# Performance work log

Hardware: AMD Instinct MI355X
Metric: run time of the kernel (lower is better)

Reference implementation:

```python
import jax, jax.numpy as jnp
import numpy as np

WIN = 9
EPS = 1e-05


def _box_sum(x, win):
    """Depthwise win x win box-filter sum with SAME padding, via two separable 1D convs."""
    C = x.shape[1]
    pad = win // 2
    dn = ('NCHW', 'OIHW', 'NCHW')
    kh = jnp.ones((C, 1, win, 1), dtype=x.dtype)
    kw = jnp.ones((C, 1, 1, win), dtype=x.dtype)
    x = jax.lax.conv_general_dilated(x, kh, (1, 1), [(pad, pad), (0, 0)],
                                     dimension_numbers=dn, feature_group_count=C)
    x = jax.lax.conv_general_dilated(x, kw, (1, 1), [(0, 0), (pad, pad)],
                                     dimension_numbers=dn, feature_group_count=C)
    return x


def setup_inputs() -> dict:
    key = jax.random.key(0)
    k1, k2 = jax.random.split(key)
    B, C, H, W = 32, 4, 512, 512
    y_pred = jax.random.uniform(k1, (B, C, H, W), dtype=jnp.float32)
    y_true = jax.random.uniform(k2, (B, C, H, W), dtype=jnp.float32)
    return {"y_pred": y_pred, "y_true": y_true}


def reference(y_pred, y_true):
    C = y_true.shape[1]
    n = float(WIN * WIN)
    # Stack the 5 moment maps along channels -> one fused box-filter pass.
    stacked = jnp.concatenate(
        [y_true, y_pred, y_true * y_true, y_pred * y_pred, y_true * y_pred], axis=1)
    sums = _box_sum(stacked, WIN)
    sum_I, sum_J, sum_I2, sum_J2, sum_IJ = jnp.split(sums, 5, axis=1)
    mu_I = sum_I / n
    mu_J = sum_J / n
    var_I = sum_I2 / n - mu_I * mu_I
    var_J = sum_J2 / n - mu_J * mu_J
    cov_IJ = sum_IJ / n - mu_I * mu_J
    cc = cov_IJ * cov_IJ / (jnp.maximum(var_I, 0.0) * jnp.maximum(var_J, 0.0) + EPS)
    return -jnp.mean(cc)
```

## Files before the change

kernel.cpp:

```cpp
#include <hip/hip_runtime.h>


#define PAD 4
#define EPS 1e-5f

constexpr int B = 32, C = 4, H = 512, W = 512;
constexpr int ROWS = 32;
constexpr int TPB = 256;
constexpr int CPT = 2;
constexpr int SLOTS = 520;
constexpr int NCHUNK = H / ROWS;
constexpr int NBLK = B * C * NCHUNK;
constexpr int NPART = NBLK * 4;
constexpr float INV_N = 1.0f / 81.0f;

template <bool ADD>
__device__ __forceinline__ void accrow(const float* __restrict__ I,
                                       const float* __restrict__ J,
                                       int r, int x0, float s[5][CPT]) {
    const float2 vi = *(const float2*)(I + (size_t)r * W + x0);
    const float2 vj = *(const float2*)(J + (size_t)r * W + x0);
    float fi[CPT] = {vi.x, vi.y};
    float fj[CPT] = {vj.x, vj.y};
#pragma unroll
    for (int k = 0; k < CPT; ++k) {
        float a = fi[k], b = fj[k];
        if (ADD) {
            s[0][k] += a; s[1][k] += b;
            s[2][k] += a * a; s[3][k] += b * b; s[4][k] += a * b;
        } else {
            s[0][k] -= a; s[1][k] -= b;
            s[2][k] -= a * a; s[3][k] -= b * b; s[4][k] -= a * b;
        }
    }
}

__global__ __launch_bounds__(TPB) void ncc_partial(
        const float* __restrict__ y_pred, const float* __restrict__ y_true,
        float* __restrict__ partial) {
    __shared__ float vs[2][5][SLOTS];

    const int bid = blockIdx.x;
    const int chunk = bid % NCHUNK;
    const int plane = bid / NCHUNK;
    const size_t base = (size_t)plane * H * W;
    const float* I = y_true + base;
    const float* J = y_pred + base;

    const int t = threadIdx.x;
    const int x0 = t * CPT;

    if (t < 2 * PAD) {
        const int sl = (t < PAD) ? t : (512 + t);
#pragma unroll
        for (int b = 0; b < 2; ++b)
#pragma unroll
            for (int ch = 0; ch < 5; ++ch) vs[b][ch][sl] = 0.0f;
    }

    const int y0 = chunk * ROWS;

    float s[5][CPT] = {{0.f, 0.f}, {0.f, 0.f}, {0.f, 0.f}, {0.f, 0.f}, {0.f, 0.f}};

    for (int r = y0 - PAD; r < y0 + PAD; ++r) {
        if (r >= 0 && r < H) accrow<true>(I, J, r, x0, s);
    }

    float acc = 0.0f;

    for (int yo = 0; yo < ROWS; ++yo) {
        const int y = y0 + yo;
        const int rin = y + PAD;
        if (rin < H) accrow<true>(I, J, rin, x0, s);

        float (* const vb)[SLOTS] = vs[yo & 1];
#pragma unroll
        for (int ch = 0; ch < 5; ++ch)
            *(float2*)&vb[ch][x0 + PAD] = make_float2(s[ch][0], s[ch][1]);
        __syncthreads();

        float h[5][CPT];
#pragma unroll
        for (int ch = 0; ch < 5; ++ch) {
            const float* row = vb[ch];
            const float2 r0 = *(const float2*)(row + x0);
            const float2 r1 = *(const float2*)(row + x0 + 2);
            const float2 r2 = *(const float2*)(row + x0 + 4);
            const float2 r3 = *(const float2*)(row + x0 + 6);
            const float2 r4 = *(const float2*)(row + x0 + 8);
            const float s0 = r0.x + r0.y + r1.x + r1.y + r2.x + r2.y +
                             r3.x + r3.y + r4.x;
            h[ch][0] = s0;
            h[ch][1] = s0 + r4.y - r0.x;
        }

#pragma unroll
        for (int k = 0; k < CPT; ++k) {
            const float mI = h[0][k] * INV_N;
            const float mJ = h[1][k] * INV_N;
            const float vI = h[2][k] * INV_N - mI * mI;
            const float vJ = h[3][k] * INV_N - mJ * mJ;
            const float cv = h[4][k] * INV_N - mI * mJ;
            const float den = fmaxf(vI, 0.0f) * fmaxf(vJ, 0.0f) + EPS;
            acc += cv * cv / den;
        }

        const int rout = y - PAD;
        if (rout >= 0) accrow<false>(I, J, rout, x0, s);
    }

#pragma unroll
    for (int off = 32; off > 0; off >>= 1)
        acc += __shfl_down(acc, off, 64);
    if ((t & 63) == 0) partial[bid * 4 + (t >> 6)] = acc;
}

__global__ __launch_bounds__(256) void ncc_final(
        const float* __restrict__ partial, float* __restrict__ out) {
    const int t = threadIdx.x;
    float sum = 0.0f;
    for (int i = t; i < NPART; i += 256) sum += partial[i];
    __shared__ float ws[4];
#pragma unroll
    for (int off = 32; off > 0; off >>= 1)
        sum += __shfl_down(sum, off, 64);
    if ((t & 63) == 0) ws[t >> 6] = sum;
    __syncthreads();
    if (t == 0) {
        const float tot = ws[0] + ws[1] + ws[2] + ws[3];
        out[0] = -tot / (float)((long long)B * C * H * W);
    }
}

extern "C" void kernel_launch(void* const* d_in, const int* in_sizes, int n_in,
                              void* d_out, int out_size, void* d_ws, size_t ws_size,
                              hipStream_t stream) {
    const float* y_pred = (const float*)d_in[0];
    const float* y_true = (const float*)d_in[1];
    float* out = (float*)d_out;
    float* partial = (float*)d_ws;

    ncc_partial<<<NBLK, TPB, 0, stream>>>(y_pred, y_true, partial);
    ncc_final<<<1, 256, 0, stream>>>(partial, out);
}
```

Measured before the change: 115.6 us.

## Map each wavefront to a row chunk, use shuffle-based horizontal box sums

Restructures the kernel so each 64-lane wavefront owns a full 512-wide row strip of 16 rows, with 8 columns per lane. The horizontal 9-tap sum now uses cross-lane shuffles instead of a shared-memory buffer, which removes the per-row __syncthreads. Row loads for the next step are issued early to overlap with compute. It also uses float4 loads, a hardware reciprocal in place of division, and a block-index swizzle across 8 groups. The costs are higher register pressure, more redundant halo row reads from the shorter chunks, and a slightly less precise reciprocal.

```diff
diff --git a/kernel.cpp b/kernel.cpp
--- a/kernel.cpp
+++ b/kernel.cpp
@@ -5,121 +5,158 @@
 #define EPS 1e-5f
 
 constexpr int B = 32, C = 4, H = 512, W = 512;
-constexpr int ROWS = 32;
+constexpr int ROWS = 16;
+constexpr int NCHUNK = H / ROWS;
+constexpr int NTASK = B * C * NCHUNK;
 constexpr int TPB = 256;
-constexpr int CPT = 2;
-constexpr int SLOTS = 520;
-constexpr int NCHUNK = H / ROWS;
-constexpr int NBLK = B * C * NCHUNK;
-constexpr int NPART = NBLK * 4;
+constexpr int WPB = TPB / 64;
+constexpr int NBLK = NTASK / WPB;
 constexpr float INV_N = 1.0f / 81.0f;
 
-template <bool ADD>
-__device__ __forceinline__ void accrow(const float* __restrict__ I,
-                                       const float* __restrict__ J,
-                                       int r, int x0, float s[5][CPT]) {
-    const float2 vi = *(const float2*)(I + (size_t)r * W + x0);
-    const float2 vj = *(const float2*)(J + (size_t)r * W + x0);
-    float fi[CPT] = {vi.x, vi.y};
-    float fj[CPT] = {vj.x, vj.y};
+__device__ __forceinline__ void loadrow(const float* __restrict__ p, int r,
+                                        int x0, float4& a, float4& b) {
+    const float* q = p + (size_t)r * W + x0;
+    a = *(const float4*)q;
+    b = *(const float4*)(q + 4);
+}
+
+__device__ __forceinline__ void unpack8(const float4& a, const float4& b,
+                                        float f[8]) {
+    f[0] = a.x; f[1] = a.y; f[2] = a.z; f[3] = a.w;
+    f[4] = b.x; f[5] = b.y; f[6] = b.z; f[7] = b.w;
+}
+
+__device__ __forceinline__ void hsum(const float sc[8], int lane, float h[8]) {
+    float L[4], R[4];
 #pragma unroll
-    for (int k = 0; k < CPT; ++k) {
-        float a = fi[k], b = fj[k];
-        if (ADD) {
-            s[0][k] += a; s[1][k] += b;
-            s[2][k] += a * a; s[3][k] += b * b; s[4][k] += a * b;
-        } else {
-            s[0][k] -= a; s[1][k] -= b;
-            s[2][k] -= a * a; s[3][k] -= b * b; s[4][k] -= a * b;
-        }
+    for (int k = 0; k < 4; ++k) {
+        L[k] = __shfl_up(sc[4 + k], 1, 64);
+        R[k] = __shfl_down(sc[k], 1, 64);
+    }
+#pragma unroll
+    for (int k = 0; k < 4; ++k) {
+        L[k] = (lane == 0) ? 0.0f : L[k];
+        R[k] = (lane == 63) ? 0.0f : R[k];
+    }
+    float w[16] = {L[0], L[1], L[2], L[3],
+                   sc[0], sc[1], sc[2], sc[3], sc[4], sc[5], sc[6], sc[7],
+                   R[0], R[1], R[2], R[3]};
+    float t = w[0] + w[1] + w[2] + w[3] + w[4] + w[5] + w[6] + w[7] + w[8];
+    h[0] = t;
+#pragma unroll
+    for (int j = 1; j < 8; ++j) {
+        t += w[j + 8] - w[j - 1];
+        h[j] = t;
     }
 }
 
-__global__ __launch_bounds__(TPB) void ncc_partial(
+__global__ __launch_bounds__(TPB, 4) void ncc_partial(
         const float* __restrict__ y_pred, const float* __restrict__ y_true,
         float* __restrict__ partial) {
-    __shared__ float vs[2][5][SLOTS];
-
-    const int bid = blockIdx.x;
-    const int chunk = bid % NCHUNK;
-    const int plane = bid / NCHUNK;
+    const int wid = threadIdx.x >> 6;
+    const int lane = threadIdx.x & 63;
+    const int g = (blockIdx.x & 7) * (NBLK / 8) + (blockIdx.x >> 3);
+    const int task = g * WPB + wid;
+    const int plane = task >> 5;
+    const int v = task & (NCHUNK - 1);
     const size_t base = (size_t)plane * H * W;
     const float* I = y_true + base;
     const float* J = y_pred + base;
+    const int x0 = lane * 8;
+    const int y0 = v * ROWS;
 
-    const int t = threadIdx.x;
-    const int x0 = t * CPT;
+    float s[5][8];
+#pragma unroll
+    for (int c = 0; c < 5; ++c)
+#pragma unroll
+        for (int k = 0; k < 8; ++k) s[c][k] = 0.0f;
 
-    if (t < 2 * PAD) {
-        const int sl = (t < PAD) ? t : (512 + t);
+    for (int r = y0 - PAD; r <= y0 + PAD; ++r) {
+        if (r < 0) continue;
+        float4 i0, i1, j0, j1;
+        loadrow(I, r, x0, i0, i1);
+        loadrow(J, r, x0, j0, j1);
+        float fi[8], fj[8];
+        unpack8(i0, i1, fi);
+        unpack8(j0, j1, fj);
 #pragma unroll
-        for (int b = 0; b < 2; ++b)
-#pragma unroll
-            for (int ch = 0; ch < 5; ++ch) vs[b][ch][sl] = 0.0f;
-    }
-
-    const int y0 = chunk * ROWS;
-
-    float s[5][CPT] = {{0.f, 0.f}, {0.f, 0.f}, {0.f, 0.f}, {0.f, 0.f}, {0.f, 0.f}};
-
-    for (int r = y0 - PAD; r < y0 + PAD; ++r) {
-        if (r >= 0 && r < H) accrow<true>(I, J, r, x0, s);
+        for (int k = 0; k < 8; ++k) {
+            const float a = fi[k], b = fj[k];
+            s[0][k] += a; s[1][k] += b;
+            s[2][k] += a * a; s[3][k] += b * b; s[4][k] += a * b;
+        }
     }
 
     float acc = 0.0f;
 
     for (int yo = 0; yo < ROWS; ++yo) {
         const int y = y0 + yo;
-        const int rin = y + PAD;
-        if (rin < H) accrow<true>(I, J, rin, x0, s);
 
-        float (* const vb)[SLOTS] = vs[yo & 1];
+        const int ra = y + PAD + 1;
+        const bool va = (yo < ROWS - 1) && (ra < H);
+        float4 ai0, ai1, aj0, aj1;
+        if (va) { loadrow(I, ra, x0, ai0, ai1); loadrow(J, ra, x0, aj0, aj1); }
+
+        float mI[8], mJ[8];
+        hsum(s[0], lane, mI);
+        hsum(s[1], lane, mJ);
+
+        const int rs = y - PAD;
+        const bool vsub = (yo < ROWS - 1) && (rs >= 0);
+        float4 si0, si1, sj0, sj1;
+        if (vsub) { loadrow(I, rs, x0, si0, si1); loadrow(J, rs, x0, sj0, sj1); }
+
+        float vI[8], vJ[8], cv[8];
+        hsum(s[2], lane, vI);
+        hsum(s[3], lane, vJ);
+        hsum(s[4], lane, cv);
+
 #pragma unroll
-        for (int ch = 0; ch < 5; ++ch)
-            *(float2*)&vb[ch][x0 + PAD] = make_float2(s[ch][0], s[ch][1]);
-        __syncthreads();
-
-        float h[5][CPT];
-#pragma unroll
-        for (int ch = 0; ch < 5; ++ch) {
-            const float* row = vb[ch];
-            const float2 r0 = *(const float2*)(row + x0);
-            const float2 r1 = *(const float2*)(row + x0 + 2);
-            const float2 r2 = *(const float2*)(row + x0 + 4);
-            const float2 r3 = *(const float2*)(row + x0 + 6);
-            const float2 r4 = *(const float2*)(row + x0 + 8);
-            const float s0 = r0.x + r0.y + r1.x + r1.y + r2.x + r2.y +
-                             r3.x + r3.y + r4.x;
-            h[ch][0] = s0;
-            h[ch][1] = s0 + r4.y - r0.x;
+        for (int k = 0; k < 8; ++k) {
+            const float mi = mI[k] * INV_N;
+            const float mj = mJ[k] * INV_N;
+            const float vi = vI[k] * INV_N - mi * mi;
+            const float vj = vJ[k] * INV_N - mj * mj;
+            const float c  = cv[k] * INV_N - mi * mj;
+            const float den = fmaxf(vi, 0.0f) * fmaxf(vj, 0.0f) + EPS;
+            acc += c * c * __builtin_amdgcn_rcpf(den);
         }
 
+        if (va) {
+            float fi[8], fj[8];
+            unpack8(ai0, ai1, fi);
+            unpack8(aj0, aj1, fj);
 #pragma unroll
-        for (int k = 0; k < CPT; ++k) {
-            const float mI = h[0][k] * INV_N;
-            const float mJ = h[1][k] * INV_N;
-            const float vI = h[2][k] * INV_N - mI * mI;
-            const float vJ = h[3][k] * INV_N - mJ * mJ;
-            const float cv = h[4][k] * INV_N - mI * mJ;
-            const float den = fmaxf(vI, 0.0f) * fmaxf(vJ, 0.0f) + EPS;
-            acc += cv * cv / den;
+            for (int k = 0; k < 8; ++k) {
+                const float a = fi[k], b = fj[k];
+                s[0][k] += a; s[1][k] += b;
+                s[2][k] += a * a; s[3][k] += b * b; s[4][k] += a * b;
+            }
         }
-
-        const int rout = y - PAD;
-        if (rout >= 0) accrow<false>(I, J, rout, x0, s);
+        if (vsub) {
+            float fi[8], fj[8];
+            unpack8(si0, si1, fi);
+            unpack8(sj0, sj1, fj);
+#pragma unroll
+            for (int k = 0; k < 8; ++k) {
+                const float a = fi[k], b = fj[k];
+                s[0][k] -= a; s[1][k] -= b;
+                s[2][k] -= a * a; s[3][k] -= b * b; s[4][k] -= a * b;
+            }
+        }
     }
 
 #pragma unroll
     for (int off = 32; off > 0; off >>= 1)
         acc += __shfl_down(acc, off, 64);
-    if ((t & 63) == 0) partial[bid * 4 + (t >> 6)] = acc;
+    if (lane == 0) partial[task] = acc;
 }
 
 __global__ __launch_bounds__(256) void ncc_final(
         const float* __restrict__ partial, float* __restrict__ out) {
     const int t = threadIdx.x;
     float sum = 0.0f;
-    for (int i = t; i < NPART; i += 256) sum += partial[i];
+    for (int i = t; i < NTASK; i += 256) sum += partial[i];
     __shared__ float ws[4];
 #pragma unroll
     for (int off = 32; off > 0; off >>= 1)
```

After: 358.0 us. 3.1x slower.
